# Optimization experiments

Hardware: AMD Instinct MI355X
Metric: run time of the kernel (lower is better)

The kernel has to match this reference:

```python
import jax, jax.numpy as jnp
import numpy as np

EPS = 1e-5

def _linear(x, w, b):
    # torch nn.Linear convention: w is [out, in]
    return jnp.einsum('...i,oi->...o', x, w) + b

def _l2_normalize(x, axis=-1):
    n = jnp.sqrt(jnp.sum(x * x, axis=axis, keepdims=True))
    return x / jnp.maximum(n, 1e-12)

def _online_softmax_scan(sim):
    # sim: [B, H, L]. Running max m_t and running sum s_t = sum_{i<=t} exp(sim_i - m_t)
    def combine(a, b):
        ma, sa = a
        mb, sb = b
        m = jnp.maximum(ma, mb)
        s = sa * jnp.exp(ma - m) + sb * jnp.exp(mb - m)
        return m, s
    m_scan, s_scan = jax.lax.associative_scan(combine, (sim, jnp.ones_like(sim)), axis=2)
    return m_scan, s_scan


def setup_inputs() -> dict:
    key = jax.random.key(0)
    ks = jax.random.split(key, 8)
    B, L, D = 2, 2048, 256
    H, h = 8, 32
    s = 1.0 / np.sqrt(D)
    inp = {
        'x': jax.random.normal(ks[0], (B, L, D), jnp.float32),
        'wq_w': jax.random.normal(ks[1], (D, D), jnp.float32) * s,
        'wq_b': jnp.zeros((D,), jnp.float32),
        'wk_w': jax.random.normal(ks[2], (D, D), jnp.float32) * s,
        'wk_b': jnp.zeros((D,), jnp.float32),
        'wv_w': jax.random.normal(ks[3], (D, D), jnp.float32) * s,
        'wv_b': jnp.zeros((D,), jnp.float32),
        'wo_w': jax.random.normal(ks[4], (D, D), jnp.float32) * s,
        'wo_b': jnp.zeros((D,), jnp.float32),
        'wg_w': jax.random.normal(ks[5], (1, h * h), jnp.float32) * (1.0 / np.sqrt(h * h)),
        'wg_b': jnp.zeros((1,), jnp.float32),
        'kv_norm_scale': jnp.ones((1, H, 1, h, h), jnp.float32),
        'qk_norm_scale': jnp.full((1, H, 1), 1.0 / np.sqrt(h), jnp.float32),
    }
    return inp


def reference(x, wq_w, wq_b, wk_w, wk_b, wv_w, wv_b, wo_w, wo_b,
              wg_w, wg_b, kv_norm_scale, qk_norm_scale):
    B, L, D = x.shape
    H, h = kv_norm_scale.shape[1], kv_norm_scale.shape[3]

    q = _linear(x, wq_w, wq_b).reshape(B, L, H, h).transpose(0, 2, 1, 3)  # bhld
    k = _linear(x, wk_w, wk_b).reshape(B, L, H, h).transpose(0, 2, 1, 3)
    v = _linear(x, wv_w, wv_b).reshape(B, L, H, h).transpose(0, 2, 1, 3)

    sim = jnp.einsum('bhld,bhld->bhl', q, k) * qk_norm_scale  # [B,H,L]

    k = _l2_normalize(k)
    v = _l2_normalize(v)

    # outer-product KV state per position: [B,H,L,h,h]
    Z = jnp.einsum('bhld,bhle->bhlde', v, k) * kv_norm_scale

    # gating: squared ReLU of linear over flattened h*h features
    gate_inputs = Z.reshape(B, H, L, h * h)
    gates_logits = jnp.einsum('bhli,oi->bhlo', gate_inputs, wg_w) + wg_b  # [B,H,L,1]
    gates = jnp.square(jax.nn.relu(gates_logits)) + EPS
    gates = gates[..., None]  # [B,H,L,1,1]
    gated_Z = gates * Z

    # associative scans along L
    m_scan, s_scan = _online_softmax_scan(sim)        # [B,H,L]
    Z_scan = jnp.cumsum(gated_Z, axis=2)              # [B,H,L,h,h]
    g_scan = jnp.cumsum(gates, axis=2)                # [B,H,L,1,1]

    softmax_weights = (jnp.exp(sim - m_scan) / (s_scan + EPS))[..., None, None]
    gated_weights = Z_scan / (g_scan + EPS)
    attn_weights = gated_weights * (1.0 + jax.nn.silu(softmax_weights))

    ctxt = jnp.einsum('bhld,bhlde->bhle', q, attn_weights)
    ctxt = ctxt.transpose(0, 2, 1, 3).reshape(B, L, D)
    return _linear(ctxt, wo_w, wo_b)
```

## Files before the change

### kernel.cpp

```cpp
#include <hip/hip_runtime.h>
#include <math.h>

#define EPSV 1e-5f

static constexpr int Ls = 2048, Hh = 8;
static constexpr int NCH = 64, T = 32;

typedef unsigned short u16;
using frag  = __attribute__((ext_vector_type(8))) short;
using f32x4 = __attribute__((ext_vector_type(4))) float;

__device__ __forceinline__ void split_bf16(float v, u16& hi, u16& lo) {
    const unsigned u = __float_as_uint(v);
    hi = (u16)(u >> 16);
    const float hf = __uint_as_float((unsigned)hi << 16);
    lo = (u16)(__float_as_uint(v - hf) >> 16);
}

__device__ __forceinline__ unsigned pk2(u16 a, u16 b) {
    return (unsigned)a | ((unsigned)b << 16);
}

__device__ __forceinline__ void split8(const float4& a, const float4& b,
                                       uint4& hi, uint4& lo) {
    u16 h[8], l[8];
    const float f[8] = {a.x, a.y, a.z, a.w, b.x, b.y, b.z, b.w};
#pragma unroll
    for (int i = 0; i < 8; ++i) split_bf16(f[i], h[i], l[i]);
    hi = make_uint4(pk2(h[0], h[1]), pk2(h[2], h[3]), pk2(h[4], h[5]), pk2(h[6], h[7]));
    lo = make_uint4(pk2(l[0], l[1]), pk2(l[2], l[3]), pk2(l[4], l[5]), pk2(l[6], l[7]));
}

__global__ __launch_bounds__(256) void qkv_fused(
    const float* __restrict__ x,
    const float* __restrict__ wq, const float* __restrict__ wk, const float* __restrict__ wv,
    const float* __restrict__ bq, const float* __restrict__ bk, const float* __restrict__ bv,
    const float* __restrict__ wg_w, const float* __restrict__ wg_b,
    const float* __restrict__ kvs, const float* __restrict__ qks,
    float* __restrict__ qh, float* __restrict__ kh, float* __restrict__ vh,
    float* __restrict__ simG, float* __restrict__ gG,
    float* __restrict__ ZcT, float* __restrict__ mT, float* __restrict__ sT,
    float* __restrict__ gTt)
{
    constexpr int LDK = 40;
    constexpr int LDT = 66;
    __shared__ __align__(16) float smemf[3 * 64 * LDT];
    __shared__ float wkS[2][1024];
    __shared__ float lsim[2][64], lg2[2][64];

    u16* As_hi = (u16*)smemf;
    u16* As_lo = As_hi + 2560;
    u16* Wst   = As_lo + 2560;
    float* Qt = smemf;
    float* Kt = Qt + 64 * LDT;
    float* Vt = Kt + 64 * LDT;

    const int tid = threadIdx.x;
    const int mt = blockIdx.x, nt = blockIdx.y;
    const int m0 = mt * 64, ncol0 = nt * 64;
    const int bidx = m0 >> 11, lg = m0 & (Ls - 1);
    const int wave = tid >> 6, lane = tid & 63;
    const int l15 = lane & 15, quad = lane >> 4;
    const int srow = tid >> 2, sk = (tid & 3) * 8;

    for (int i = tid; i < 2048; i += 256) {
        const int h = i >> 10, de = i & 1023;
        wkS[h][de] = wg_w[de] * kvs[(nt * 2 + h) * 1024 + de];
    }

    const float* Wsrc[3] = {wq, wk, wv};
    f32x4 acc[3][4] = {};

    for (int k0 = 0; k0 < 256; k0 += 32) {
        const float4 a0 = *(const float4*)&x[(size_t)(m0 + srow) * 256 + k0 + sk];
        const float4 a1 = *(const float4*)&x[(size_t)(m0 + srow) * 256 + k0 + sk + 4];
        float4 w0[3], w1[3];
#pragma unroll
        for (int w = 0; w < 3; ++w) {
            w0[w] = *(const float4*)&Wsrc[w][(size_t)(ncol0 + srow) * 256 + k0 + sk];
            w1[w] = *(const float4*)&Wsrc[w][(size_t)(ncol0 + srow) * 256 + k0 + sk + 4];
        }
        __syncthreads();
        {
            uint4 hi, lo;
            split8(a0, a1, hi, lo);
            *(uint4*)&As_hi[srow * LDK + sk] = hi;
            *(uint4*)&As_lo[srow * LDK + sk] = lo;
#pragma unroll
            for (int w = 0; w < 3; ++w) {
                split8(w0[w], w1[w], hi, lo);
                *(uint4*)&Wst[w * 5120 + srow * LDK + sk] = hi;
                *(uint4*)&Wst[w * 5120 + 2560 + srow * LDK + sk] = lo;
            }
        }
        __syncthreads();

        const frag ah = *(const frag*)&As_hi[(wave * 16 + l15) * LDK + quad * 8];
        const frag al = *(const frag*)&As_lo[(wave * 16 + l15) * LDK + quad * 8];
#pragma unroll
        for (int w = 0; w < 3; ++w)
#pragma unroll
            for (int cf = 0; cf < 4; ++cf) {
                const u16* bp = &Wst[w * 5120 + (cf * 16 + l15) * LDK + quad * 8];
                const frag bh = *(const frag*)bp;
                const frag bl = *(const frag*)(bp + 2560);
                acc[w][cf] = __builtin_amdgcn_mfma_f32_16x16x32_bf16(ah, bh, acc[w][cf], 0, 0, 0);
                acc[w][cf] = __builtin_amdgcn_mfma_f32_16x16x32_bf16(ah, bl, acc[w][cf], 0, 0, 0);
                acc[w][cf] = __builtin_amdgcn_mfma_f32_16x16x32_bf16(al, bh, acc[w][cf], 0, 0, 0);
            }
    }
    __syncthreads();

    {
        float* tiles[3] = {Qt, Kt, Vt};
        const float* biases[3] = {bq, bk, bv};
#pragma unroll
        for (int w = 0; w < 3; ++w)
#pragma unroll
            for (int cf = 0; cf < 4; ++cf) {
                const int col = cf * 16 + l15;
                const float bias = biases[w][ncol0 + col];
#pragma unroll
                for (int r = 0; r < 4; ++r) {
                    const int m = wave * 16 + quad * 4 + r;
                    tiles[w][m * LDT + col] = acc[w][cf][r] + bias;
                }
            }
    }
    __syncthreads();

    if (tid < 128) {
        const int h = tid >> 6, l = tid & 63;
        const int cb = h * 32;
        float ksum = 0.f, vsum = 0.f, qk = 0.f;
#pragma unroll 8
        for (int e = 0; e < 32; ++e) {
            const float kv = Kt[l * LDT + cb + e];
            const float vv = Vt[l * LDT + cb + e];
            const float qv = Qt[l * LDT + cb + e];
            ksum = fmaf(kv, kv, ksum);
            vsum = fmaf(vv, vv, vsum);
            qk = fmaf(qv, kv, qk);
        }
        const float kscale = 1.f / fmaxf(sqrtf(ksum), 1e-12f);
        const float vscale = 1.f / fmaxf(sqrtf(vsum), 1e-12f);
#pragma unroll 8
        for (int e = 0; e < 32; ++e) {
            Kt[l * LDT + cb + e] *= kscale;
            Vt[l * LDT + cb + e] *= vscale;
        }
        const float sim = qk * qks[nt * 2 + h];
        lsim[h][l] = sim;
        simG[(size_t)(bidx * 8 + nt * 2 + h) * Ls + lg + l] = sim;
    }
    __syncthreads();

    {
        const float* tl[3] = {Qt, Kt, Vt};
        float* gl[3] = {qh, kh, vh};
#pragma unroll
        for (int arr = 0; arr < 3; ++arr)
#pragma unroll
            for (int it = 0; it < 8; ++it) {
                const int idx = it * 512 + tid * 2;
                const int h = idx >> 11, rem = idx & 2047;
                const int l = rem >> 5, e = rem & 31;
                float2 v;
                v.x = tl[arr][l * LDT + h * 32 + e];
                v.y = tl[arr][l * LDT + h * 32 + e + 1];
                *(float2*)&gl[arr][(size_t)(bidx * 8 + nt * 2 + h) * 65536 +
                                   (size_t)(lg + l) * 32 + e] = v;
            }
    }

    {
        const int task = tid >> 1, half = tid & 1;
        const int h = task >> 6, l = task & 63;
        float vreg[32];
#pragma unroll 8
        for (int d = 0; d < 32; ++d) vreg[d] = Vt[l * LDT + h * 32 + d];
        float u = 0.f;
        const int e0 = half * 16;
#pragma unroll 4
        for (int e = e0; e < e0 + 16; ++e) {
            float s = 0.f;
#pragma unroll 8
            for (int d = 0; d < 32; ++d)
                s = fmaf(vreg[d], wkS[h][d * 32 + e], s);
            u = fmaf(s, Kt[l * LDT + h * 32 + e], u);
        }
        u += __shfl_xor(u, 1);
        if (half == 0) {
            const float r = fmaxf(u + wg_b[0], 0.f);
            const float g = r * r + EPSV;
            lg2[h][l] = g;
            gG[(size_t)(bidx * 8 + nt * 2 + h) * Ls + lg + l] = g;
        }
    }
    __syncthreads();

    {
        const int d = tid >> 3, e0 = (tid & 7) * 4;
#pragma unroll
        for (int h = 0; h < 2; ++h)
#pragma unroll
            for (int cc = 0; cc < 2; ++cc) {
                float z0 = 0.f, z1 = 0.f, z2 = 0.f, z3 = 0.f;
#pragma unroll 8
                for (int l = 0; l < 32; ++l) {
                    const int lr = cc * 32 + l;
                    const float gv = lg2[h][lr] * Vt[lr * LDT + h * 32 + d];
                    z0 = fmaf(gv, Kt[lr * LDT + h * 32 + e0 + 0], z0);
                    z1 = fmaf(gv, Kt[lr * LDT + h * 32 + e0 + 1], z1);
                    z2 = fmaf(gv, Kt[lr * LDT + h * 32 + e0 + 2], z2);
                    z3 = fmaf(gv, Kt[lr * LDT + h * 32 + e0 + 3], z3);
                }
                const int bhg = bidx * 8 + nt * 2 + h;
                const int cg = (lg >> 5) + cc;
                float4 zv; zv.x = z0; zv.y = z1; zv.z = z2; zv.w = z3;
                *(float4*)&ZcT[((size_t)bhg * NCH + cg) * 1024 + d * 32 + e0] = zv;
            }
    }

    {
        const int h = wave >> 1, cc = wave & 1;
        if (lane < 32) {
            const int lr = cc * 32 + lane;
            float m = lsim[h][lr], s = 1.f, g = lg2[h][lr];
#pragma unroll
            for (int off = 16; off; off >>= 1) {
                const float mo = __shfl_xor(m, off);
                const float so = __shfl_xor(s, off);
                const float mn = fmaxf(m, mo);
                s = s * __expf(m - mn) + so * __expf(mo - mn);
                m = mn;
                g += __shfl_xor(g, off);
            }
            if (lane == 0) {
                const int bhg = bidx * 8 + nt * 2 + h;
                const int cg = (lg >> 5) + cc;
                mT[bhg * NCH + cg] = m;
                sT[bhg * NCH + cg] = s;
                gTt[bhg * NCH + cg] = g;
            }
        }
    }
}

__global__ __launch_bounds__(256) void prefix_kernel(
    float* __restrict__ Zc, float* __restrict__ mT, float* __restrict__ sT,
    float* __restrict__ gTt,
    const float* __restrict__ kvs, float* __restrict__ aW, float* __restrict__ bW,
    int* __restrict__ flagW)
{
    const int bh = blockIdx.x, seg = blockIdx.y;
    const int tid = threadIdx.x;
    const int el = seg * 256 + tid;
    float* Zb = Zc + (size_t)bh * NCH * 1024 + el;

    float run = 0.f;
#pragma unroll
    for (int cb = 0; cb < NCH; cb += 8) {
        float v[8];
#pragma unroll
        for (int i = 0; i < 8; ++i) v[i] = Zb[(size_t)(cb + i) * 1024];
#pragma unroll
        for (int i = 0; i < 8; ++i) {
            const float t = v[i];
            Zb[(size_t)(cb + i) * 1024] = run;
            run += t;
        }
    }

    if (seg == 0 && tid < 64) {
        float m = mT[bh * NCH + tid], s = sT[bh * NCH + tid], g = gTt[bh * NCH + tid];
#pragma unroll
        for (int off = 1; off < 64; off <<= 1) {
            const float mo = __shfl_up(m, off);
            const float so = __shfl_up(s, off);
            const float go = __shfl_up(g, off);
            if (tid >= off) {
                const float mn = fmaxf(m, mo);
                s = s * __expf(m - mn) + so * __expf(mo - mn);
                m = mn;
                g += go;
            }
        }
        float me = __shfl_up(m, 1), se = __shfl_up(s, 1), ge = __shfl_up(g, 1);
        if (tid == 0) { me = -1e30f; se = 0.f; ge = 0.f; }
        mT[bh * NCH + tid] = me;
        sT[bh * NCH + tid] = se;
        gTt[bh * NCH + tid] = ge;
    }

    if (bh == 0 && seg == 3) {
        const int h = tid >> 5, e = tid & 31;
        const float* K = kvs + h * 1024;
        const float k00 = K[0];
        int ok = (k00 != 0.0f);
        for (int d = 0; d < 32; ++d) {
            const float lhs = K[d * 32 + e] * k00;
            const float rhs = K[d * 32] * K[e];
            const float diff = fabsf(lhs - rhs);
            if (diff > 1e-6f * fmaxf(fmaxf(fabsf(lhs), fabsf(rhs)), 1e-20f)) ok = 0;
        }
        aW[h * 32 + e] = K[e * 32];
        bW[h * 32 + e] = (k00 != 0.0f) ? K[e] / k00 : 0.f;
        const int allok = __syncthreads_and(ok);
        if (tid == 0) flagW[0] = allok;
    }
}

__global__ __launch_bounds__(1024) void chunk_out_kernel(
    const float* __restrict__ qh, const float* __restrict__ knG, const float* __restrict__ vnG,
    const float* __restrict__ simG, const float* __restrict__ gG,
    const float* __restrict__ kvs,
    const float* __restrict__ ZcP, const float* __restrict__ mP,
    const float* __restrict__ sP, const float* __restrict__ gP,
    const float* __restrict__ aW, const float* __restrict__ bW,
    const int* __restrict__ flagW,
    u16* __restrict__ chi, u16* __restrict__ clo)
{
    __shared__ float qa[1024], knb[1024], zp[1024], lkvs[1024];
    __shared__ float vnT[32 * 33], sW[32 * 33];
    __shared__ float la[32], lb[32], lg[T], lsim[T], lwgt[T];
    const int tid = threadIdx.x;
    const int c = blockIdx.x, bh = blockIdx.y, h = bh & 7, b = bh >> 3;
    const int l = tid >> 5, lane = tid & 31;
    const size_t base = ((size_t)bh * Ls + c * T) * 32;
    const int flag = flagW[0];

    const float qv = qh[base + tid];
    const float knv = knG[base + tid];
    const float vnv = vnG[base + tid];
    vnT[lane * 33 + l] = vnv;
    zp[tid] = ZcP[((size_t)bh * NCH + c) * 1024 + tid];
    if (!flag) lkvs[tid] = kvs[h * 1024 + tid];
    if (tid < 32) {
        la[tid] = aW[h * 32 + tid];
        lb[tid] = bW[h * 32 + tid];
        lg[tid] = gG[bh * Ls + c * T + tid];
        lsim[tid] = simG[bh * Ls + c * T + tid];
    }
    __syncthreads();

    qa[tid] = flag ? qv * la[lane] : qv;
    knb[tid] = flag ? knv * lb[lane] : knv;
    if (tid < 32) {
        float m = lsim[tid], s = 1.f, g = lg[tid];
#pragma unroll
        for (int off = 1; off < 32; off <<= 1) {
            const float mo = __shfl_up(m, off);
            const float so = __shfl_up(s, off);
            const float go = __shfl_up(g, off);
            if (tid >= off) {
                const float mn = fmaxf(m, mo);
                s = s * __expf(m - mn) + so * __expf(mo - mn);
                m = mn;
                g += go;
            }
        }
        const float mp = mP[bh * NCH + c];
        const float sp = sP[bh * NCH + c];
        const float gp = gP[bh * NCH + c];
        const float mn = fmaxf(mp, m);
        s = sp * __expf(mp - mn) + s * __expf(m - mn);
        m = mn;
        g += gp;
        const float sw = __expf(lsim[tid] - m) / (s + EPSV);
        const float sig = 1.f / (1.f + __expf(-sw));
        lwgt[tid] = (1.f + sw * sig) / (g + EPSV);
    }
    __syncthreads();

    float y;
    if (flag) {
        float s = 0.f, y0 = 0.f;
        const float4* qa4 = (const float4*)&qa[l * 32];
#pragma unroll
        for (int d4 = 0; d4 < 8; ++d4) {
            const float4 q4 = qa4[d4];
            const int d = d4 * 4;
            s = fmaf(q4.x, vnT[(d + 0) * 33 + lane], s);
            s = fmaf(q4.y, vnT[(d + 1) * 33 + lane], s);
            s = fmaf(q4.z, vnT[(d + 2) * 33 + lane], s);
            s = fmaf(q4.w, vnT[(d + 3) * 33 + lane], s);
            y0 = fmaf(q4.x, zp[(d + 0) * 32 + lane], y0);
            y0 = fmaf(q4.y, zp[(d + 1) * 32 + lane], y0);
            y0 = fmaf(q4.z, zp[(d + 2) * 32 + lane], y0);
            y0 = fmaf(q4.w, zp[(d + 3) * 32 + lane], y0);
        }
        sW[l * 33 + lane] = (lane <= l) ? lg[lane] * s : 0.f;
        __syncthreads();
        y = y0 * lb[lane];
#pragma unroll 8
        for (int j = 0; j < 32; ++j)
            y = fmaf(sW[l * 33 + j], knb[j * 32 + lane], y);
        y *= lwgt[l];
    } else {
        float qe[32];
#pragma unroll
        for (int d = 0; d < 32; ++d)
            qe[d] = qa[l * 32 + d] * lkvs[d * 32 + lane];
        y = 0.f;
#pragma unroll
        for (int d = 0; d < 32; ++d)
            y = fmaf(qe[d], zp[d * 32 + lane], y);
        for (int j = 0; j < 32; ++j) {
            float s = 0.f;
#pragma unroll
            for (int d = 0; d < 32; ++d)
                s = fmaf(qe[d], vnT[d * 33 + j], s);
            if (j <= l) y = fmaf(lg[j] * s, knb[j * 32 + lane], y);
        }
        y *= lwgt[l];
    }
    u16 hi, lo;
    split_bf16(y, hi, lo);
    const size_t oidx = ((size_t)(b * Ls + c * T + l)) * 256 + h * 32 + lane;
    chi[oidx] = hi;
    clo[oidx] = lo;
}

__global__ __launch_bounds__(256) void out_gemm(
    const u16* __restrict__ Ahi, const u16* __restrict__ Alo,
    const float* __restrict__ wo, const float* __restrict__ bo,
    float* __restrict__ out)
{
    constexpr int LDK = 40;
    __shared__ __align__(16) u16 As_hi[64 * LDK];
    __shared__ __align__(16) u16 As_lo[64 * LDK];
    __shared__ __align__(16) u16 Ws_hi[64 * LDK];
    __shared__ __align__(16) u16 Ws_lo[64 * LDK];

    const int tid = threadIdx.x;
    const int mt = blockIdx.x, nt = blockIdx.y;
    const int m0 = mt * 64, ncol0 = nt * 64;
    const int wave = tid >> 6, lane = tid & 63;
    const int l15 = lane & 15, quad = lane >> 4;
    const int srow = tid >> 2, sk = (tid & 3) * 8;

    f32x4 acc[4] = {};

    for (int k0 = 0; k0 < 256; k0 += 32) {
        const uint4 ah = *(const uint4*)&Ahi[(size_t)(m0 + srow) * 256 + k0 + sk];
        const uint4 al = *(const uint4*)&Alo[(size_t)(m0 + srow) * 256 + k0 + sk];
        const float4 w0 = *(const float4*)&wo[(size_t)(ncol0 + srow) * 256 + k0 + sk];
        const float4 w1 = *(const float4*)&wo[(size_t)(ncol0 + srow) * 256 + k0 + sk + 4];
        __syncthreads();
        uint4 whi, wlo;
        split8(w0, w1, whi, wlo);
        *(uint4*)&As_hi[srow * LDK + sk] = ah;
        *(uint4*)&As_lo[srow * LDK + sk] = al;
        *(uint4*)&Ws_hi[srow * LDK + sk] = whi;
        *(uint4*)&Ws_lo[srow * LDK + sk] = wlo;
        __syncthreads();

        const frag fah = *(const frag*)&As_hi[(wave * 16 + l15) * LDK + quad * 8];
        const frag fal = *(const frag*)&As_lo[(wave * 16 + l15) * LDK + quad * 8];
#pragma unroll
        for (int cf = 0; cf < 4; ++cf) {
            const frag fbh = *(const frag*)&Ws_hi[(cf * 16 + l15) * LDK + quad * 8];
            const frag fbl = *(const frag*)&Ws_lo[(cf * 16 + l15) * LDK + quad * 8];
            acc[cf] = __builtin_amdgcn_mfma_f32_16x16x32_bf16(fah, fbh, acc[cf], 0, 0, 0);
            acc[cf] = __builtin_amdgcn_mfma_f32_16x16x32_bf16(fah, fbl, acc[cf], 0, 0, 0);
            acc[cf] = __builtin_amdgcn_mfma_f32_16x16x32_bf16(fal, fbh, acc[cf], 0, 0, 0);
        }
    }

#pragma unroll
    for (int cf = 0; cf < 4; ++cf) {
        const int o = ncol0 + cf * 16 + l15;
        const float bias = bo[o];
#pragma unroll
        for (int r = 0; r < 4; ++r) {
            const int rm = m0 + wave * 16 + quad * 4 + r;
            out[(size_t)rm * 256 + o] = acc[cf][r] + bias;
        }
    }
}

extern "C" void kernel_launch(void* const* d_in, const int* in_sizes, int n_in,
                              void* d_out, int out_size, void* d_ws, size_t ws_size,
                              hipStream_t stream) {
    const float* x    = (const float*)d_in[0];
    const float* wq_w = (const float*)d_in[1];
    const float* wq_b = (const float*)d_in[2];
    const float* wk_w = (const float*)d_in[3];
    const float* wk_b = (const float*)d_in[4];
    const float* wv_w = (const float*)d_in[5];
    const float* wv_b = (const float*)d_in[6];
    const float* wo_w = (const float*)d_in[7];
    const float* wo_b = (const float*)d_in[8];
    const float* wg_w = (const float*)d_in[9];
    const float* wg_b = (const float*)d_in[10];
    const float* kvs  = (const float*)d_in[11];
    const float* qks  = (const float*)d_in[12];
    float* out = (float*)d_out;

    u16* chi = (u16*)d_ws;
    u16* clo = chi + 1048576;
    float* qh   = (float*)(clo + 1048576);
    float* kh   = qh + 1048576;
    float* vh   = kh + 1048576;
    float* ZcT  = vh + 1048576;
    float* simG = ZcT + 1048576;
    float* gG   = simG + 32768;
    float* mT   = gG + 32768;
    float* sT   = mT + 1024;
    float* gTt  = sT + 1024;
    float* aW   = gTt + 1024;
    float* bW   = aW + 256;
    int* flagW  = (int*)(bW + 256);

    qkv_fused<<<dim3(64, 4), 256, 0, stream>>>(
        x, wq_w, wk_w, wv_w, wq_b, wk_b, wv_b, wg_w, wg_b, kvs, qks,
        qh, kh, vh, simG, gG, ZcT, mT, sT, gTt);
    prefix_kernel<<<dim3(16, 4), 256, 0, stream>>>(
        ZcT, mT, sT, gTt, kvs, aW, bW, flagW);
    chunk_out_kernel<<<dim3(NCH, 16), 1024, 0, stream>>>(
        qh, kh, vh, simG, gG, kvs, ZcT, mT, sT, gTt, aW, bW, flagW, chi, clo);
    out_gemm<<<dim3(64, 4), 256, 0, stream>>>(
        chi, clo, wo_w, wo_b, out);
}
```

Measured before the change: 145.2 us.

## Vectorize LDS access, parallelize chunk prefix scan, and shrink chunk_out blocks

The fused QKV kernel now reads and writes its LDS tiles with float4 accesses. It pads the tile stride to 68 and transposes the gate weight matrix so the gate dot products can be vectorized. The chunk prefix kernel runs 4x more blocks, each doing a shared-memory Hillis-Steele scan over 64 chunks instead of one serial loop per thread. chunk_out_kernel drops from 1024 to 256 threads, with each thread computing four output columns via float4 loads, which raises per-thread work and register pressure but cuts LDS traffic.

```diff
diff --git a/kernel.cpp b/kernel.cpp
--- a/kernel.cpp
+++ b/kernel.cpp
@@ -43,9 +43,9 @@
     float* __restrict__ gTt)
 {
     constexpr int LDK = 40;
-    constexpr int LDT = 66;
+    constexpr int LDT = 68;
     __shared__ __align__(16) float smemf[3 * 64 * LDT];
-    __shared__ float wkS[2][1024];
+    __shared__ __align__(16) float wkT[2][32 * 36];
     __shared__ float lsim[2][64], lg2[2][64];
 
     u16* As_hi = (u16*)smemf;
@@ -65,7 +65,8 @@
 
     for (int i = tid; i < 2048; i += 256) {
         const int h = i >> 10, de = i & 1023;
-        wkS[h][de] = wg_w[de] * kvs[(nt * 2 + h) * 1024 + de];
+        const int d = de >> 5, e = de & 31;
+        wkT[h][e * 36 + d] = wg_w[de] * kvs[(nt * 2 + h) * 1024 + de];
     }
 
     const float* Wsrc[3] = {wq, wk, wv};
@@ -131,23 +132,27 @@
 
     if (tid < 128) {
         const int h = tid >> 6, l = tid & 63;
-        const int cb = h * 32;
+        const int rb = l * LDT + h * 32;
+        float4 kr[8], vr[8];
         float ksum = 0.f, vsum = 0.f, qk = 0.f;
-#pragma unroll 8
-        for (int e = 0; e < 32; ++e) {
-            const float kv = Kt[l * LDT + cb + e];
-            const float vv = Vt[l * LDT + cb + e];
-            const float qv = Qt[l * LDT + cb + e];
-            ksum = fmaf(kv, kv, ksum);
-            vsum = fmaf(vv, vv, vsum);
-            qk = fmaf(qv, kv, qk);
+#pragma unroll
+        for (int e4 = 0; e4 < 8; ++e4) {
+            kr[e4] = *(const float4*)&Kt[rb + e4 * 4];
+            vr[e4] = *(const float4*)&Vt[rb + e4 * 4];
+            const float4 q4 = *(const float4*)&Qt[rb + e4 * 4];
+            ksum += kr[e4].x * kr[e4].x + kr[e4].y * kr[e4].y + kr[e4].z * kr[e4].z + kr[e4].w * kr[e4].w;
+            vsum += vr[e4].x * vr[e4].x + vr[e4].y * vr[e4].y + vr[e4].z * vr[e4].z + vr[e4].w * vr[e4].w;
+            qk   += q4.x * kr[e4].x + q4.y * kr[e4].y + q4.z * kr[e4].z + q4.w * kr[e4].w;
         }
         const float kscale = 1.f / fmaxf(sqrtf(ksum), 1e-12f);
         const float vscale = 1.f / fmaxf(sqrtf(vsum), 1e-12f);
-#pragma unroll 8
-        for (int e = 0; e < 32; ++e) {
-            Kt[l * LDT + cb + e] *= kscale;
-            Vt[l * LDT + cb + e] *= vscale;
+#pragma unroll
+        for (int e4 = 0; e4 < 8; ++e4) {
+            float4 k4 = kr[e4], v4 = vr[e4];
+            k4.x *= kscale; k4.y *= kscale; k4.z *= kscale; k4.w *= kscale;
+            v4.x *= vscale; v4.y *= vscale; v4.z *= vscale; v4.w *= vscale;
+            *(float4*)&Kt[rb + e4 * 4] = k4;
+            *(float4*)&Vt[rb + e4 * 4] = v4;
         }
         const float sim = qk * qks[nt * 2 + h];
         lsim[h][l] = sim;
@@ -161,33 +166,37 @@
 #pragma unroll
         for (int arr = 0; arr < 3; ++arr)
 #pragma unroll
-            for (int it = 0; it < 8; ++it) {
-                const int idx = it * 512 + tid * 2;
+            for (int it = 0; it < 4; ++it) {
+                const int idx = it * 1024 + tid * 4;
                 const int h = idx >> 11, rem = idx & 2047;
-                const int l = rem >> 5, e = rem & 31;
-                float2 v;
-                v.x = tl[arr][l * LDT + h * 32 + e];
-                v.y = tl[arr][l * LDT + h * 32 + e + 1];
-                *(float2*)&gl[arr][(size_t)(bidx * 8 + nt * 2 + h) * 65536 +
-                                   (size_t)(lg + l) * 32 + e] = v;
+                const int l = rem >> 5, e4 = rem & 31;
+                const float4 v = *(const float4*)&tl[arr][l * LDT + h * 32 + e4];
+                *(float4*)&gl[arr][(size_t)(bidx * 8 + nt * 2 + h) * 65536 +
+                                   (size_t)(lg + l) * 32 + e4] = v;
             }
     }
 
     {
         const int task = tid >> 1, half = tid & 1;
         const int h = task >> 6, l = task & 63;
-        float vreg[32];
-#pragma unroll 8
-        for (int d = 0; d < 32; ++d) vreg[d] = Vt[l * LDT + h * 32 + d];
+        float4 vr[8];
+#pragma unroll
+        for (int d4 = 0; d4 < 8; ++d4)
+            vr[d4] = *(const float4*)&Vt[l * LDT + h * 32 + d4 * 4];
         float u = 0.f;
         const int e0 = half * 16;
 #pragma unroll 4
         for (int e = e0; e < e0 + 16; ++e) {
-            float s = 0.f;
-#pragma unroll 8
-            for (int d = 0; d < 32; ++d)
-                s = fmaf(vreg[d], wkS[h][d * 32 + e], s);
-            u = fmaf(s, Kt[l * LDT + h * 32 + e], u);
+            float4 s4 = make_float4(0.f, 0.f, 0.f, 0.f);
+#pragma unroll
+            for (int d4 = 0; d4 < 8; ++d4) {
+                const float4 w4 = *(const float4*)&wkT[h][e * 36 + d4 * 4];
+                s4.x = fmaf(vr[d4].x, w4.x, s4.x);
+                s4.y = fmaf(vr[d4].y, w4.y, s4.y);
+                s4.z = fmaf(vr[d4].z, w4.z, s4.z);
+                s4.w = fmaf(vr[d4].w, w4.w, s4.w);
+            }
+            u = fmaf(s4.x + s4.y + s4.z + s4.w, Kt[l * LDT + h * 32 + e], u);
         }
         u += __shfl_xor(u, 1);
         if (half == 0) {
@@ -200,25 +209,25 @@
     __syncthreads();
 
     {
-        const int d = tid >> 3, e0 = (tid & 7) * 4;
+        const int d = tid >> 3, e4m = (tid & 7) * 4;
 #pragma unroll
         for (int h = 0; h < 2; ++h)
 #pragma unroll
             for (int cc = 0; cc < 2; ++cc) {
-                float z0 = 0.f, z1 = 0.f, z2 = 0.f, z3 = 0.f;
+                float4 z4 = make_float4(0.f, 0.f, 0.f, 0.f);
 #pragma unroll 8
                 for (int l = 0; l < 32; ++l) {
                     const int lr = cc * 32 + l;
                     const float gv = lg2[h][lr] * Vt[lr * LDT + h * 32 + d];
-                    z0 = fmaf(gv, Kt[lr * LDT + h * 32 + e0 + 0], z0);
-                    z1 = fmaf(gv, Kt[lr * LDT + h * 32 + e0 + 1], z1);
-                    z2 = fmaf(gv, Kt[lr * LDT + h * 32 + e0 + 2], z2);
-                    z3 = fmaf(gv, Kt[lr * LDT + h * 32 + e0 + 3], z3);
+                    const float4 k4 = *(const float4*)&Kt[lr * LDT + h * 32 + e4m];
+                    z4.x = fmaf(gv, k4.x, z4.x);
+                    z4.y = fmaf(gv, k4.y, z4.y);
+                    z4.z = fmaf(gv, k4.z, z4.z);
+                    z4.w = fmaf(gv, k4.w, z4.w);
                 }
                 const int bhg = bidx * 8 + nt * 2 + h;
                 const int cg = (lg >> 5) + cc;
-                float4 zv; zv.x = z0; zv.y = z1; zv.z = z2; zv.w = z3;
-                *(float4*)&ZcT[((size_t)bhg * NCH + cg) * 1024 + d * 32 + e0] = zv;
+                *(float4*)&ZcT[((size_t)bhg * NCH + cg) * 1024 + d * 32 + e4m] = z4;
             }
     }
 
@@ -253,23 +262,36 @@
     const float* __restrict__ kvs, float* __restrict__ aW, float* __restrict__ bW,
     int* __restrict__ flagW)
 {
+    __shared__ float sc[64 * 64];
     const int bh = blockIdx.x, seg = blockIdx.y;
     const int tid = threadIdx.x;
-    const int el = seg * 256 + tid;
-    float* Zb = Zc + (size_t)bh * NCH * 1024 + el;
-
-    float run = 0.f;
-#pragma unroll
-    for (int cb = 0; cb < NCH; cb += 8) {
-        float v[8];
-#pragma unroll
-        for (int i = 0; i < 8; ++i) v[i] = Zb[(size_t)(cb + i) * 1024];
-#pragma unroll
-        for (int i = 0; i < 8; ++i) {
-            const float t = v[i];
-            Zb[(size_t)(cb + i) * 1024] = run;
-            run += t;
-        }
+    float* Zb = Zc + (size_t)bh * NCH * 1024 + seg * 64;
+
+#pragma unroll
+    for (int it = 0; it < 16; ++it) {
+        const int idx = it * 256 + tid;
+        const int cc = idx >> 6, e = idx & 63;
+        sc[idx] = Zb[(size_t)cc * 1024 + e];
+    }
+    __syncthreads();
+#pragma unroll
+    for (int st = 1; st < 64; st <<= 1) {
+        float tmp[16];
+#pragma unroll
+        for (int it = 0; it < 16; ++it) {
+            const int idx = it * 256 + tid;
+            tmp[it] = ((idx >> 6) >= st) ? sc[idx - st * 64] : 0.f;
+        }
+        __syncthreads();
+#pragma unroll
+        for (int it = 0; it < 16; ++it) sc[it * 256 + tid] += tmp[it];
+        __syncthreads();
+    }
+#pragma unroll
+    for (int it = 0; it < 16; ++it) {
+        const int idx = it * 256 + tid;
+        const int cc = idx >> 6, e = idx & 63;
+        Zb[(size_t)cc * 1024 + e] = cc ? sc[idx - 64] : 0.f;
     }
 
     if (seg == 0 && tid < 64) {
@@ -293,7 +315,7 @@
         gTt[bh * NCH + tid] = ge;
     }
 
-    if (bh == 0 && seg == 3) {
+    if (bh == 0 && seg == 1) {
         const int h = tid >> 5, e = tid & 31;
         const float* K = kvs + h * 1024;
         const float k00 = K[0];
@@ -311,7 +333,7 @@
     }
 }
 
-__global__ __launch_bounds__(1024) void chunk_out_kernel(
+__global__ __launch_bounds__(256) void chunk_out_kernel(
     const float* __restrict__ qh, const float* __restrict__ knG, const float* __restrict__ vnG,
     const float* __restrict__ simG, const float* __restrict__ gG,
     const float* __restrict__ kvs,
@@ -321,33 +343,47 @@
     const int* __restrict__ flagW,
     u16* __restrict__ chi, u16* __restrict__ clo)
 {
-    __shared__ float qa[1024], knb[1024], zp[1024], lkvs[1024];
-    __shared__ float vnT[32 * 33], sW[32 * 33];
-    __shared__ float la[32], lb[32], lg[T], lsim[T], lwgt[T];
+    __shared__ __align__(16) float qa[1024], knb[1024], zp[1024], sW[1024];
+    __shared__ __align__(16) float vnT[32 * 36];
+    __shared__ float lkvs[1024];
+    __shared__ float lgS[32], lsimS[32], lwgt[32];
     const int tid = threadIdx.x;
     const int c = blockIdx.x, bh = blockIdx.y, h = bh & 7, b = bh >> 3;
-    const int l = tid >> 5, lane = tid & 31;
-    const size_t base = ((size_t)bh * Ls + c * T) * 32;
+    const int l = tid >> 3, e4 = (tid & 7) * 4;
+    const size_t base4 = ((size_t)bh * Ls + (size_t)c * T) * 8 + tid;
     const int flag = flagW[0];
 
-    const float qv = qh[base + tid];
-    const float knv = knG[base + tid];
-    const float vnv = vnG[base + tid];
-    vnT[lane * 33 + l] = vnv;
-    zp[tid] = ZcP[((size_t)bh * NCH + c) * 1024 + tid];
-    if (!flag) lkvs[tid] = kvs[h * 1024 + tid];
+    const float4 qv4 = ((const float4*)qh)[base4];
+    const float4 kn4 = ((const float4*)knG)[base4];
+    const float4 vn4 = ((const float4*)vnG)[base4];
+    const float4 z4  = ((const float4*)ZcP)[((size_t)bh * NCH + c) * 256 + tid];
+    const float4 la4 = *(const float4*)&aW[h * 32 + e4];
+    const float4 lb4 = *(const float4*)&bW[h * 32 + e4];
     if (tid < 32) {
-        la[tid] = aW[h * 32 + tid];
-        lb[tid] = bW[h * 32 + tid];
-        lg[tid] = gG[bh * Ls + c * T + tid];
-        lsim[tid] = simG[bh * Ls + c * T + tid];
+        lgS[tid] = gG[bh * Ls + c * T + tid];
+        lsimS[tid] = simG[bh * Ls + c * T + tid];
+    }
+    if (!flag) {
+        *(float4*)&lkvs[tid * 4] = *(const float4*)&kvs[h * 1024 + tid * 4];
+    }
+    {
+        float4 q = qv4, k = kn4;
+        if (flag) {
+            q.x *= la4.x; q.y *= la4.y; q.z *= la4.z; q.w *= la4.w;
+            k.x *= lb4.x; k.y *= lb4.y; k.z *= lb4.z; k.w *= lb4.w;
+        }
+        *(float4*)&qa[l * 32 + e4] = q;
+        *(float4*)&knb[l * 32 + e4] = k;
+        *(float4*)&zp[tid * 4] = z4;
+        vnT[(e4 + 0) * 36 + l] = vn4.x;
+        vnT[(e4 + 1) * 36 + l] = vn4.y;
+        vnT[(e4 + 2) * 36 + l] = vn4.z;
+        vnT[(e4 + 3) * 36 + l] = vn4.w;
     }
     __syncthreads();
 
-    qa[tid] = flag ? qv * la[lane] : qv;
-    knb[tid] = flag ? knv * lb[lane] : knv;
     if (tid < 32) {
-        float m = lsim[tid], s = 1.f, g = lg[tid];
+        float m = lsimS[tid], s = 1.f, g = lgS[tid];
 #pragma unroll
         for (int off = 1; off < 32; off <<= 1) {
             const float mo = __shfl_up(m, off);
@@ -367,59 +403,87 @@
         s = sp * __expf(mp - mn) + s * __expf(m - mn);
         m = mn;
         g += gp;
-        const float sw = __expf(lsim[tid] - m) / (s + EPSV);
+        const float sw = __expf(lsimS[tid] - m) / (s + EPSV);
         const float sig = 1.f / (1.f + __expf(-sw));
         lwgt[tid] = (1.f + sw * sig) / (g + EPSV);
     }
-    __syncthreads();
-
-    float y;
+
+    float4 y4 = make_float4(0.f, 0.f, 0.f, 0.f);
     if (flag) {
-        float s = 0.f, y0 = 0.f;
-        const float4* qa4 = (const float4*)&qa[l * 32];
-#pragma unroll
-        for (int d4 = 0; d4 < 8; ++d4) {
-            const float4 q4 = qa4[d4];
-            const int d = d4 * 4;
-            s = fmaf(q4.x, vnT[(d + 0) * 33 + lane], s);
-            s = fmaf(q4.y, vnT[(d + 1) * 33 + lane], s);
-            s = fmaf(q4.z, vnT[(d + 2) * 33 + lane], s);
-            s = fmaf(q4.w, vnT[(d + 3) * 33 + lane], s);
-            y0 = fmaf(q4.x, zp[(d + 0) * 32 + lane], y0);
-            y0 = fmaf(q4.y, zp[(d + 1) * 32 + lane], y0);
-            y0 = fmaf(q4.z, zp[(d + 2) * 32 + lane], y0);
-            y0 = fmaf(q4.w, zp[(d + 3) * 32 + lane], y0);
-        }
-        sW[l * 33 + lane] = (lane <= l) ? lg[lane] * s : 0.f;
-        __syncthreads();
-        y = y0 * lb[lane];
+        float qrow[32];
+#pragma unroll
+        for (int d4 = 0; d4 < 8; ++d4)
+            *(float4*)&qrow[d4 * 4] = *(const float4*)&qa[l * 32 + d4 * 4];
+        float4 s4 = make_float4(0.f, 0.f, 0.f, 0.f);
 #pragma unroll 8
-        for (int j = 0; j < 32; ++j)
-            y = fmaf(sW[l * 33 + j], knb[j * 32 + lane], y);
-        y *= lwgt[l];
+        for (int d = 0; d < 32; ++d) {
+            const float qd = qrow[d];
+            const float4 v4 = *(const float4*)&vnT[d * 36 + e4];
+            const float4 p4 = *(const float4*)&zp[d * 32 + e4];
+            s4.x = fmaf(qd, v4.x, s4.x);
+            s4.y = fmaf(qd, v4.y, s4.y);
+            s4.z = fmaf(qd, v4.z, s4.z);
+            s4.w = fmaf(qd, v4.w, s4.w);
+            y4.x = fmaf(qd, p4.x, y4.x);
+            y4.y = fmaf(qd, p4.y, y4.y);
+            y4.z = fmaf(qd, p4.z, y4.z);
+            y4.w = fmaf(qd, p4.w, y4.w);
+        }
+        y4.x *= lb4.x; y4.y *= lb4.y; y4.z *= lb4.z; y4.w *= lb4.w;
+        const float4 lg4 = *(const float4*)&lgS[e4];
+        float4 sm;
+        sm.x = (e4 + 0 <= l) ? lg4.x * s4.x : 0.f;
+        sm.y = (e4 + 1 <= l) ? lg4.y * s4.y : 0.f;
+        sm.z = (e4 + 2 <= l) ? lg4.z * s4.z : 0.f;
+        sm.w = (e4 + 3 <= l) ? lg4.w * s4.w : 0.f;
+        *(float4*)&sW[l * 32 + e4] = sm;
+        __syncthreads();
+        float srow[32];
+#pragma unroll
+        for (int j4 = 0; j4 < 8; ++j4)
+            *(float4*)&srow[j4 * 4] = *(const float4*)&sW[l * 32 + j4 * 4];
+#pragma unroll 8
+        for (int j = 0; j < 32; ++j) {
+            const float sj = srow[j];
+            const float4 k4 = *(const float4*)&knb[j * 32 + e4];
+            y4.x = fmaf(sj, k4.x, y4.x);
+            y4.y = fmaf(sj, k4.y, y4.y);
+            y4.z = fmaf(sj, k4.z, y4.z);
+            y4.w = fmaf(sj, k4.w, y4.w);
+        }
     } else {
-        float qe[32];
-#pragma unroll
-        for (int d = 0; d < 32; ++d)
-            qe[d] = qa[l * 32 + d] * lkvs[d * 32 + lane];
-        y = 0.f;
-#pragma unroll
-        for (int d = 0; d < 32; ++d)
-            y = fmaf(qe[d], zp[d * 32 + lane], y);
-        for (int j = 0; j < 32; ++j) {
-            float s = 0.f;
+        __syncthreads();
+        float* yp = &y4.x;
+#pragma unroll
+        for (int i = 0; i < 4; ++i) {
+            const int e = e4 + i;
+            float qe[32];
 #pragma unroll
             for (int d = 0; d < 32; ++d)
-                s = fmaf(qe[d], vnT[d * 33 + j], s);
-            if (j <= l) y = fmaf(lg[j] * s, knb[j * 32 + lane], y);
-        }
-        y *= lwgt[l];
-    }
-    u16 hi, lo;
-    split_bf16(y, hi, lo);
-    const size_t oidx = ((size_t)(b * Ls + c * T + l)) * 256 + h * 32 + lane;
-    chi[oidx] = hi;
-    clo[oidx] = lo;
+                qe[d] = qa[l * 32 + d] * lkvs[d * 32 + e];
+            float y = 0.f;
+#pragma unroll
+            for (int d = 0; d < 32; ++d)
+                y = fmaf(qe[d], zp[d * 32 + e], y);
+            for (int j = 0; j < 32; ++j) {
+                float s = 0.f;
+#pragma unroll
+                for (int d = 0; d < 32; ++d)
+                    s = fmaf(qe[d], vnT[d * 36 + j], s);
+                if (j <= l) y = fmaf(lgS[j] * s, knb[j * 32 + e], y);
+            }
+            yp[i] = y;
+        }
+    }
+    const float w = lwgt[l];
+    ushort4 hi4, lo4;
+    split_bf16(y4.x * w, hi4.x, lo4.x);
+    split_bf16(y4.y * w, hi4.y, lo4.y);
+    split_bf16(y4.z * w, hi4.z, lo4.z);
+    split_bf16(y4.w * w, hi4.w, lo4.w);
+    const size_t oidx = ((size_t)(b * Ls + c * T + l)) * 256 + h * 32 + e4;
+    *(ushort4*)&chi[oidx] = hi4;
+    *(ushort4*)&clo[oidx] = lo4;
 }
 
 __global__ __launch_bounds__(256) void out_gemm(
@@ -516,9 +580,9 @@
     qkv_fused<<<dim3(64, 4), 256, 0, stream>>>(
         x, wq_w, wk_w, wv_w, wq_b, wk_b, wv_b, wg_w, wg_b, kvs, qks,
         qh, kh, vh, simG, gG, ZcT, mT, sT, gTt);
-    prefix_kernel<<<dim3(16, 4), 256, 0, stream>>>(
+    prefix_kernel<<<dim3(16, 16), 256, 0, stream>>>(
         ZcT, mT, sT, gTt, kvs, aW, bW, flagW);
-    chunk_out_kernel<<<dim3(NCH, 16), 1024, 0, stream>>>(
+    chunk_out_kernel<<<dim3(NCH, 16), 256, 0, stream>>>(
         qh, kh, vh, simG, gG, kvs, ZcT, mT, sT, gTt, aW, bW, flagW, chi, clo);
     out_gemm<<<dim3(64, 4), 256, 0, stream>>>(
         chi, clo, wo_w, wo_b, out);
```

New measurement: 157.6 us. 8.5% more time.
